# Performance work log

Measured on AMD Instinct MI355X. Metric: run time of the kernel, lower is better.

## Reference

```python
import jax, jax.numpy as jnp
import numpy as np
from jax import lax

B, S, D, H, K = 2, 2048, 1024, 16, 3  # batch, seq, embed, heads, conv kernel
DEPTH = D // H


def silu(x):
    return x * jax.nn.sigmoid(x)


def sep_conv1d(x, dw, pw, b):
    """Keras SeparableConv1D, padding='same', activation=silu.
    x: [B,S,C]; dw: [K,1,C] depthwise kernel; pw: [C,F] pointwise; b: [F]."""
    C = x.shape[-1]
    y = lax.conv_general_dilated(
        x, dw, window_strides=(1,), padding='SAME',
        dimension_numbers=('NWC', 'WIO', 'NWC'), feature_group_count=C)
    y = jnp.einsum('bsc,cf->bsf', y, pw) + b
    return silu(y)


def setup_inputs() -> dict:
    key = jax.random.key(0)
    ks = jax.random.split(key, 20)
    sc = 1.0 / np.sqrt(D)
    inp = {
        'v': jax.random.normal(ks[0], (B, S, D), jnp.float32),
        'k': jax.random.normal(ks[1], (B, S, D), jnp.float32),
        'q': jax.random.normal(ks[2], (B, S, D), jnp.float32),
        'mask': jax.random.randint(ks[3], (B, 1, 1, S), 0, 2, jnp.int32),
        # Dense wq/wk/wv (SiLU)
        'wq_w': jax.random.normal(ks[4], (D, D), jnp.float32) * sc,
        'wq_b': jnp.zeros((D,), jnp.float32),
        'wk_w': jax.random.normal(ks[5], (D, D), jnp.float32) * sc,
        'wk_b': jnp.zeros((D,), jnp.float32),
        'wv_w': jax.random.normal(ks[6], (D, D), jnp.float32) * sc,
        'wv_b': jnp.zeros((D,), jnp.float32),
        # SeparableConv1D params (depthwise [K,1,D], pointwise [D,D], bias [D])
        'dwq': jax.random.normal(ks[7], (K, 1, D), jnp.float32) * 0.1,
        'pwq': jax.random.normal(ks[8], (D, D), jnp.float32) * sc,
        'bq': jnp.zeros((D,), jnp.float32),
        'dwk': jax.random.normal(ks[9], (K, 1, D), jnp.float32) * 0.1,
        'pwk': jax.random.normal(ks[10], (D, D), jnp.float32) * sc,
        'bk': jnp.zeros((D,), jnp.float32),
        'dwv': jax.random.normal(ks[11], (K, 1, D), jnp.float32) * 0.1,
        'pwv': jax.random.normal(ks[12], (D, D), jnp.float32) * sc,
        'bv': jnp.zeros((D,), jnp.float32),
        # output Dense (SiLU)
        'wo_w': jax.random.normal(ks[13], (D, D), jnp.float32) * sc,
        'wo_b': jnp.zeros((D,), jnp.float32),
    }
    return inp


def reference(v, k, q, mask, wq_w, wq_b, wk_w, wk_b, wv_w, wv_b,
              dwq, pwq, bq, dwk, pwk, bk, dwv, pwv, bv, wo_w, wo_b):
    # Dense projections with SiLU
    qp = silu(q @ wq_w + wq_b)
    kp = silu(k @ wk_w + wk_b)
    vp = silu(v @ wv_w + wv_b)
    # SeparableConv1D enhancements (SiLU)
    qc = sep_conv1d(qp, dwq, pwq, bq)
    kc = sep_conv1d(kp, dwk, pwk, bk)
    vc = sep_conv1d(vp, dwv, pwv, bv)
    # split heads -> [B,H,S,depth]
    def split(x):
        return x.reshape(B, S, H, DEPTH).transpose(0, 2, 1, 3)
    qh, kh, vh = split(qc), split(kc), split(vc)
    # scaled dot-product attention with additive mask penalty
    logits = jnp.einsum('bhqd,bhkd->bhqk', qh, kh) / jnp.sqrt(jnp.float32(DEPTH))
    logits = logits + mask.astype(jnp.float32) * -1e9
    attn = jax.nn.softmax(logits, axis=-1)
    out = jnp.einsum('bhqk,bhkd->bhqd', attn, vh)
    out = out.transpose(0, 2, 1, 3).reshape(B, S, D)
    return silu(out @ wo_w + wo_b)
```

## Files before the change

### kernel.cpp

```cpp
#include <hip/hip_runtime.h>
#include <hip/hip_fp16.h>
#include <math.h>

#define BB 2
#define SS 2048
#define DD 1024
#define HH 16
#define MTOT (BB*SS)

typedef _Float16 f16;
typedef _Float16 f16x4 __attribute__((ext_vector_type(4)));
typedef _Float16 f16x8 __attribute__((ext_vector_type(8)));
typedef float    f32x4 __attribute__((ext_vector_type(4)));

#define KSCALE 0.1803368801111204f

__device__ __forceinline__ float silu_f(float x) {
    return x / (1.0f + __expf(-x));
}

__device__ __forceinline__ void gload16(void* lds, const void* g) {
    __builtin_amdgcn_global_load_lds(
        (const __attribute__((address_space(1))) unsigned*)g,
        (__attribute__((address_space(3))) unsigned*)lds, 16, 0, 0);
}

__global__ __launch_bounds__(256) void prep(
    const float* __restrict__ q, const float* __restrict__ k, const float* __restrict__ v,
    f16* __restrict__ x0, f16* __restrict__ x1, f16* __restrict__ x2,
    const float* __restrict__ w0, const float* __restrict__ w1, const float* __restrict__ w2,
    const float* __restrict__ w3, const float* __restrict__ w4, const float* __restrict__ w5,
    const float* __restrict__ w6, f16* __restrict__ wt,
    const int* __restrict__ mask, int* __restrict__ uidx, int* __restrict__ ucnt)
{
    __shared__ float ts[64][65];
    const int gid = blockIdx.x;
    const int t = threadIdx.x;

    if (gid < 6144) {
        const int z = gid >> 11;
        const float* src = z == 0 ? q : z == 1 ? k : v;
        f16* dst = z == 0 ? x0 : z == 1 ? x1 : x2;
        const size_t i8 = ((size_t)(gid & 2047) * 256 + t) * 8;
        const float4 a = *(const float4*)(src + i8);
        const float4 b = *(const float4*)(src + i8 + 4);
        f16x8 h = {(f16)a.x,(f16)a.y,(f16)a.z,(f16)a.w,(f16)b.x,(f16)b.y,(f16)b.z,(f16)b.w};
        *(f16x8*)(dst + i8) = h;
    } else if (gid < 7936) {
        const int w = gid - 6144;
        const int z = w >> 8;
        const int rem = w & 255;
        const int bn = (rem & 15) << 6, bk = (rem >> 4) << 6;
        const float* src;
        switch (z) {
            case 0: src = w0; break; case 1: src = w1; break;
            case 2: src = w2; break; case 3: src = w3; break;
            case 4: src = w4; break; case 5: src = w5; break;
            default: src = w6; break;
        }
        f16* dst = wt + ((size_t)z << 20);
        #pragma unroll
        for (int i = 0; i < 4; ++i) {
            const int fid = t + (i << 8);
            const int r = fid >> 4, c4 = (fid & 15) << 2;
            const float4 v4 = *(const float4*)(src + (size_t)(bk + r) * 1024 + bn + c4);
            ts[r][c4 + 0] = v4.x; ts[r][c4 + 1] = v4.y;
            ts[r][c4 + 2] = v4.z; ts[r][c4 + 3] = v4.w;
        }
        __syncthreads();
        #pragma unroll
        for (int i = 0; i < 4; ++i) {
            const int fid = t + (i << 8);
            const int nr = fid >> 4, k4 = (fid & 15) << 2;
            f16x4 h = { (f16)ts[k4 + 0][nr], (f16)ts[k4 + 1][nr],
                        (f16)ts[k4 + 2][nr], (f16)ts[k4 + 3][nr] };
            *(f16x4*)(dst + (size_t)(bn + nr) * 1024 + bk + k4) = h;
        }
    } else {
        int* ps = (int*)ts;
        const int b = gid - 7936;
        int f[8]; int cnt = 0;
        const int base = b * SS + t * 8;
        #pragma unroll
        for (int j = 0; j < 8; ++j) { f[j] = (mask[base + j] == 0); cnt += f[j]; }
        ps[t] = cnt;
        __syncthreads();
        for (int off = 1; off < 256; off <<= 1) {
            const int pv = (t >= off) ? ps[t - off] : 0;
            __syncthreads();
            ps[t] += pv;
            __syncthreads();
        }
        int pos = ps[t] - cnt;
        #pragma unroll
        for (int j = 0; j < 8; ++j)
            if (f[j]) uidx[b * SS + pos++] = t * 8 + j;
        const int total = ps[255];
        const int pad = (total + 63) & ~63;
        for (int j = total + t; j < pad; j += 256) uidx[b * SS + j] = 0;
        if (t == 0) { ucnt[b * 2] = total; ucnt[b * 2 + 1] = pad; }
    }
}

__global__ __launch_bounds__(256) void dwconv3g(
    const f16* __restrict__ p0, const f16* __restrict__ p1, const f16* __restrict__ p2,
    const float* __restrict__ w0, const float* __restrict__ w1, const float* __restrict__ w2,
    f16* __restrict__ o0, f16* __restrict__ o1, f16* __restrict__ o2)
{
    const int z = blockIdx.y;
    const f16* x = z == 0 ? p0 : z == 1 ? p1 : p2;
    const float* dw = z == 0 ? w0 : z == 1 ? w1 : w2;
    f16* y = z == 0 ? o0 : z == 1 ? o1 : o2;
    const size_t i8 = ((size_t)blockIdx.x * 256 + threadIdx.x) * 8;
    const int c = (int)(i8 % DD);
    const int s = (int)((i8 / DD) % SS);
    const f16x8 xc = *(const f16x8*)(x + i8);
    float acc[8];
    #pragma unroll
    for (int j = 0; j < 8; ++j) acc[j] = (float)xc[j] * dw[DD + c + j];
    if (s > 0) {
        const f16x8 xm = *(const f16x8*)(x + i8 - DD);
        #pragma unroll
        for (int j = 0; j < 8; ++j) acc[j] = fmaf((float)xm[j], dw[c + j], acc[j]);
    }
    if (s < SS - 1) {
        const f16x8 xp = *(const f16x8*)(x + i8 + DD);
        #pragma unroll
        for (int j = 0; j < 8; ++j) acc[j] = fmaf((float)xp[j], dw[2 * DD + c + j], acc[j]);
    }
    f16x8 o;
    #pragma unroll
    for (int j = 0; j < 8; ++j) o[j] = (f16)acc[j];
    *(f16x8*)(y + i8) = o;
}

struct GArg { const f16* A; const f16* W; const float* b; void* C; float scale; };

template<int OUTF32>
__global__ __launch_bounds__(256) void gemm_f16(GArg g0, GArg g1, GArg g2)
{
    __shared__ f16 As[128 * 64];
    __shared__ f16 Bs[128 * 64];

    const GArg ga = blockIdx.z == 0 ? g0 : blockIdx.z == 1 ? g1 : g2;
    const int t = threadIdx.x, l = t & 63, wv = t >> 6;
    const int lr = l & 15, lg = l >> 4;
    const int wr = wv >> 1, wc = wv & 1;

    const int bid = blockIdx.y * 8 + blockIdx.x;
    const int sw = (bid & 7) * 32 + (bid >> 3);
    const int brow = (sw >> 3) << 7, bcol = (sw & 7) << 7;

    const int srow = l >> 3;
    const int schk = (l & 7) ^ (l >> 3);
    const f16* Abase = ga.A + (size_t)(brow + wv * 32 + srow) * 1024 + schk * 8;
    const f16* Bbase = ga.W + (size_t)(bcol + wv * 32 + srow) * 1024 + schk * 8;

    f32x4 acc[4][4];
    #pragma unroll
    for (int m = 0; m < 4; ++m)
        #pragma unroll
        for (int n = 0; n < 4; ++n) acc[m][n] = (f32x4){0.f, 0.f, 0.f, 0.f};

    for (int kt = 0; kt < 16; ++kt) {
        const int k0 = kt << 6;
        #pragma unroll
        for (int j = 0; j < 4; ++j) {
            gload16(As + (wv * 4 + j) * 512, Abase + (size_t)j * 8 * 1024 + k0);
            gload16(Bs + (wv * 4 + j) * 512, Bbase + (size_t)j * 8 * 1024 + k0);
        }
        __syncthreads();

        #pragma unroll
        for (int kk = 0; kk < 2; ++kk) {
            f16x8 af[4], bf[4];
            #pragma unroll
            for (int m = 0; m < 4; ++m) {
                const int row = (wr << 6) + (m << 4) + lr;
                const int off = row * 128 + ((((kk << 6) | (lg << 4))) ^ ((lr & 7) << 4));
                af[m] = *(const f16x8*)((const char*)As + off);
            }
            #pragma unroll
            for (int n = 0; n < 4; ++n) {
                const int row = (wc << 6) + (n << 4) + lr;
                const int off = row * 128 + ((((kk << 6) | (lg << 4))) ^ ((lr & 7) << 4));
                bf[n] = *(const f16x8*)((const char*)Bs + off);
            }
            #pragma unroll
            for (int m = 0; m < 4; ++m)
                #pragma unroll
                for (int n = 0; n < 4; ++n)
                    acc[m][n] = __builtin_amdgcn_mfma_f32_16x16x32_f16(af[m], bf[n], acc[m][n], 0, 0, 0);
        }
        __syncthreads();
    }

    float bv[4];
    #pragma unroll
    for (int n = 0; n < 4; ++n) bv[n] = ga.b[bcol + (wc << 6) + (n << 4) + lr];
    #pragma unroll
    for (int m = 0; m < 4; ++m)
        #pragma unroll
        for (int n = 0; n < 4; ++n)
            #pragma unroll
            for (int i = 0; i < 4; ++i) {
                const int row = brow + (wr << 6) + (m << 4) + (lg << 2) + i;
                const int col = bcol + (wc << 6) + (n << 4) + lr;
                const float o = silu_f(acc[m][n][i] + bv[n]) * ga.scale;
                if (OUTF32) ((float*)ga.C)[(size_t)row * 1024 + col] = o;
                else        ((f16*)ga.C)[(size_t)row * 1024 + col] = (f16)o;
            }
}

__global__ __launch_bounds__(512) void gemm256(GArg g0, GArg g1, GArg g2)
{
    __shared__ f16 As[256 * 64];
    __shared__ f16 Bs[128 * 64];

    const GArg ga = blockIdx.z == 0 ? g0 : blockIdx.z == 1 ? g1 : g2;
    const int t = threadIdx.x, l = t & 63, wv = t >> 6;
    const int lr = l & 15, lg = l >> 4;
    const int wm = wv >> 1, wn = wv & 1;

    const int bid = blockIdx.y * 8 + blockIdx.x;
    const int sw = (bid & 7) * 16 + (bid >> 3);
    const int brow = (sw >> 3) << 8;
    const int bcol = (sw & 7) << 7;

    const int srow = l >> 3;
    const int schk = (l & 7) ^ (l >> 3);
    const f16* Abase = ga.A + (size_t)(brow + wv * 32 + srow) * 1024 + schk * 8;
    const f16* Bbase = ga.W + (size_t)(bcol + wv * 16 + srow) * 1024 + schk * 8;

    f32x4 acc[4][4];
    #pragma unroll
    for (int m = 0; m < 4; ++m)
        #pragma unroll
        for (int n = 0; n < 4; ++n) acc[m][n] = (f32x4){0.f, 0.f, 0.f, 0.f};

    for (int kt = 0; kt < 16; ++kt) {
        const int k0 = kt << 6;
        #pragma unroll
        for (int j = 0; j < 4; ++j)
            gload16(As + (wv * 4 + j) * 512, Abase + (size_t)j * 8 * 1024 + k0);
        #pragma unroll
        for (int j = 0; j < 2; ++j)
            gload16(Bs + (wv * 2 + j) * 512, Bbase + (size_t)j * 8 * 1024 + k0);
        __syncthreads();

        #pragma unroll
        for (int kk = 0; kk < 2; ++kk) {
            f16x8 af[4], bf[4];
            #pragma unroll
            for (int m = 0; m < 4; ++m) {
                const int row = (wm << 6) + (m << 4) + lr;
                const int off = row * 128 + ((((kk << 6) | (lg << 4))) ^ ((lr & 7) << 4));
                af[m] = *(const f16x8*)((const char*)As + off);
            }
            #pragma unroll
            for (int n = 0; n < 4; ++n) {
                const int row = (wn << 6) + (n << 4) + lr;
                const int off = row * 128 + ((((kk << 6) | (lg << 4))) ^ ((lr & 7) << 4));
                bf[n] = *(const f16x8*)((const char*)Bs + off);
            }
            #pragma unroll
            for (int m = 0; m < 4; ++m)
                #pragma unroll
                for (int n = 0; n < 4; ++n)
                    acc[m][n] = __builtin_amdgcn_mfma_f32_16x16x32_f16(af[m], bf[n], acc[m][n], 0, 0, 0);
        }
        __syncthreads();
    }

    float bv[4];
    #pragma unroll
    for (int n = 0; n < 4; ++n) bv[n] = ga.b[bcol + (wn << 6) + (n << 4) + lr];
    #pragma unroll
    for (int m = 0; m < 4; ++m)
        #pragma unroll
        for (int n = 0; n < 4; ++n)
            #pragma unroll
            for (int i = 0; i < 4; ++i) {
                const int row = brow + (wm << 6) + (m << 4) + (lg << 2) + i;
                const int col = bcol + (wn << 6) + (n << 4) + lr;
                const float o = silu_f(acc[m][n][i] + bv[n]) * ga.scale;
                ((f16*)ga.C)[(size_t)row * 1024 + col] = (f16)o;
            }
}

__global__ __launch_bounds__(512) void attn_f16(
    const f16* __restrict__ Q, const f16* __restrict__ Kf,
    const f16* __restrict__ Vf, const int* __restrict__ uidx,
    const int* __restrict__ ucnt, f16* __restrict__ O)
{
    __shared__ f16 Ks[2 * 64 * 64];
    __shared__ f16 Vt[2 * 64 * 64];
    __shared__ f16 Pw[8 * 16 * 64];
    __shared__ int uix[2048];

    const int t = threadIdx.x;
    const int l = t & 63, wv = t >> 6;
    const int lr = l & 15, lg = l >> 4;

    const int bid = blockIdx.x;
    const int sw = (bid & 7) * 64 + (bid >> 3);
    const int qb = (sw & 15) << 7;
    const int h  = (sw >> 4) & 15;
    const int b  = sw >> 8;

    const int cnt = ucnt[b * 2];
    const int pad = ucnt[b * 2 + 1];

    const int srow = l >> 3;
    const int schk = (l & 7) ^ (l >> 3);

    const int bkv = (t & 15) << 2;
    const int bnv = (t >> 4) << 2;

    for (int j = t; j < 2048; j += 512) uix[j] = uidx[b * SS + j];

    const size_t bbase = (size_t)b * SS;
    const size_t qrow = bbase + qb + (wv << 4) + lr;
    const f16x8 aq0 = *(const f16x8*)(Q + qrow * DD + h * 64 + (lg << 3));
    const f16x8 aq1 = *(const f16x8*)(Q + qrow * DD + h * 64 + 32 + (lg << 3));

    float m_s = -1e30f, l_s = 0.f;
    f32x4 acc[4];
    #pragma unroll
    for (int n = 0; n < 4; ++n) acc[n] = (f32x4){0.f, 0.f, 0.f, 0.f};

    const int rdswz = (lr & 7) << 4;
    const int poff = (wv << 11) + lr * 128;

    __syncthreads();

#define PROCESS(TB, KT) do {                                                  \
    const int kb = (TB) * 8192;                                               \
    f16x8 bk0[4], bk1[4];                                                     \
    _Pragma("unroll")                                                         \
    for (int n = 0; n < 4; ++n) {                                             \
        const int row = (n << 4) + lr;                                        \
        bk0[n] = *(const f16x8*)((const char*)Ks + kb + row * 128 + (((lg << 4)) ^ rdswz));        \
        bk1[n] = *(const f16x8*)((const char*)Ks + kb + row * 128 + (((64) | (lg << 4)) ^ rdswz)); \
    }                                                                         \
    const bool full = ((KT) + 64 <= cnt);                                     \
                 \
    f32x4 s[4];                                                               \
    __builtin_amdgcn_s_setprio(1);                                            \
    _Pragma("unroll")                                                         \
    for (int n = 0; n < 4; ++n) {                                             \
        f32x4 z = (f32x4){0.f, 0.f, 0.f, 0.f};                                \
        z = __builtin_amdgcn_mfma_f32_16x16x32_f16(bk0[n], aq0, z, 0, 0, 0);  \
        z = __builtin_amdgcn_mfma_f32_16x16x32_f16(bk1[n], aq1, z, 0, 0, 0);  \
        if (full) {                                                           \
            _Pragma("unroll")                                                 \
            for (int i = 0; i < 4; ++i) s[n][i] = z[i];                       \
        } else {                                                              \
            _Pragma("unroll")                                                 \
            for (int i = 0; i < 4; ++i) {                                     \
                const bool valid = ((KT) + (n << 4) + (lg << 2) + i) < cnt;   \
                s[n][i] = valid ? z[i] : -1e30f;                              \
            }                                                                 \
        }                                                                     \
    }                                                                         \
    __builtin_amdgcn_s_setprio(0);                                            \
                   \
    float pm = s[0][0];                                                       \
    _Pragma("unroll")                                                         \
    for (int n = 0; n < 4; ++n)                                               \
        _Pragma("unroll")                                                     \
        for (int i = 0; i < 4; ++i) pm = fmaxf(pm, s[n][i]);                  \
    if (!__all(pm - m_s <= 8.0f)) {           \
        float pr = pm;                                                        \
        pr = fmaxf(pr, __shfl_xor(pr, 16));                                   \
        pr = fmaxf(pr, __shfl_xor(pr, 32));                                   \
        const float mn = fmaxf(m_s, pr);                                      \
        const float sc = exp2f(m_s - mn);                                     \
        m_s = mn;                                                             \
        l_s *= sc;                                                            \
        _Pragma("unroll")                                                     \
        for (int n = 0; n < 4; ++n)                                           \
            _Pragma("unroll")                                                 \
            for (int i = 0; i < 4; ++i) acc[n][i] *= sc;                      \
    }                                                                         \
      \
    _Pragma("unroll")                                                         \
    for (int n = 0; n < 4; ++n) {                                             \
        f16x4 p4;                                                             \
        _Pragma("unroll")                                                     \
        for (int i = 0; i < 4; ++i) {                                         \
            const float p = exp2f(s[n][i] - m_s);         \
            l_s += p;                                                         \
            p4[i] = (f16)p;                                                   \
        }                                                                     \
        const int off = poff + (((n << 5) | (lg << 3)) ^ rdswz);              \
        *(f16x4*)((char*)Pw + off) = p4;                                      \
    }                                                                         \
             \
    {                                                                         \
        const f16x8 pb0 = *(const f16x8*)((const char*)Pw + poff + (((lg << 4)) ^ rdswz));        \
        const f16x8 pb1 = *(const f16x8*)((const char*)Pw + poff + (((64) | (lg << 4)) ^ rdswz)); \
        __builtin_amdgcn_s_setprio(1);                                        \
        _Pragma("unroll")                                                     \
        for (int n = 0; n < 4; ++n) {                                         \
            const int row = (n << 4) + lr;                                    \
            const f16x8 av0 = *(const f16x8*)((const char*)Vt + kb + row * 128 + (((lg << 4)) ^ rdswz));        \
            const f16x8 av1 = *(const f16x8*)((const char*)Vt + kb + row * 128 + (((64) | (lg << 4)) ^ rdswz)); \
            acc[n] = __builtin_amdgcn_mfma_f32_16x16x32_f16(av0, pb0, acc[n], 0, 0, 0);  \
            acc[n] = __builtin_amdgcn_mfma_f32_16x16x32_f16(av1, pb1, acc[n], 0, 0, 0);  \
        }                                                                     \
        __builtin_amdgcn_s_setprio(0);                                        \
    }                                                                         \
} while (0)

    for (int kt = 0; kt < pad; kt += 128) {
        const bool two = (kt + 64) < pad;
        {
            const int krow0 = uix[kt + wv * 8 + srow];
            gload16(Ks + wv * 512, Kf + (bbase + krow0) * DD + h * 64 + schk * 8);
            if (two) {
                const int krow1 = uix[kt + 64 + wv * 8 + srow];
                gload16(Ks + 4096 + wv * 512, Kf + (bbase + krow1) * DD + h * 64 + schk * 8);
            }
        }
        if (t < 256) {
            const int nhalf = two ? 2 : 1;
            for (int half = 0; half < nhalf; ++half) {
                f16x4 vl[4];
                #pragma unroll
                for (int r = 0; r < 4; ++r) {
                    const int vrow = uix[kt + half * 64 + bkv + r];
                    vl[r] = *(const f16x4*)(Vf + (bbase + vrow) * DD + h * 64 + bnv);
                }
                #pragma unroll
                for (int j = 0; j < 4; ++j) {
                    f16x4 h4 = { vl[0][j], vl[1][j], vl[2][j], vl[3][j] };
                    const int row = bnv + j;
                    const int off = half * 8192 + row * 128 + ((bkv * 2) ^ ((row & 7) << 4));
                    *(f16x4*)((char*)Vt + off) = h4;
                }
            }
        }
        __syncthreads();

        PROCESS(0, kt);
        if (two) PROCESS(1, kt + 64);

        __syncthreads();
    }
#undef PROCESS

    l_s += __shfl_xor(l_s, 16);
    l_s += __shfl_xor(l_s, 32);
    const float inv = 1.0f / l_s;
    const size_t orow = bbase + qb + (wv << 4) + lr;
    #pragma unroll
    for (int n = 0; n < 4; ++n) {
        f16x4 o4;
        #pragma unroll
        for (int i = 0; i < 4; ++i) o4[i] = (f16)(acc[n][i] * inv);
        *(f16x4*)(O + orow * DD + h * 64 + (n << 4) + (lg << 2)) = o4;
    }
}

extern "C" void kernel_launch(void* const* d_in, const int* in_sizes, int n_in,
                              void* d_out, int out_size, void* d_ws, size_t ws_size,
                              hipStream_t stream) {
    const float* v    = (const float*)d_in[0];
    const float* k    = (const float*)d_in[1];
    const float* q    = (const float*)d_in[2];
    const int*   mask = (const int*)  d_in[3];
    const float* wq_w = (const float*)d_in[4];
    const float* wq_b = (const float*)d_in[5];
    const float* wk_w = (const float*)d_in[6];
    const float* wk_b = (const float*)d_in[7];
    const float* wv_w = (const float*)d_in[8];
    const float* wv_b = (const float*)d_in[9];
    const float* dwq  = (const float*)d_in[10];
    const float* pwq  = (const float*)d_in[11];
    const float* bq   = (const float*)d_in[12];
    const float* dwk  = (const float*)d_in[13];
    const float* pwk  = (const float*)d_in[14];
    const float* bk   = (const float*)d_in[15];
    const float* dwv  = (const float*)d_in[16];
    const float* pwv  = (const float*)d_in[17];
    const float* bv   = (const float*)d_in[18];
    const float* wo_w = (const float*)d_in[19];
    const float* wo_b = (const float*)d_in[20];
    float* out = (float*)d_out;

    const size_t NE = (size_t)MTOT * DD;
    f16* wt = (f16*)d_ws;
    f16* x0 = wt + 7 * (size_t)(1 << 20);
    f16* x1 = x0 + NE;
    f16* x2 = x1 + NE;
    f16* p0 = x2 + NE;
    f16* p1 = p0 + NE;
    f16* p2 = p1 + NE;
    f16* ao = p2 + NE;
    int* uidx = (int*)(ao + NE);
    int* ucnt = uidx + MTOT;

    f16* wtq = wt,              *wtk = wt + (1u<<20), *wtv = wt + 2*(1u<<20);
    f16* wpq = wt + 3*(1u<<20), *wpk = wt + 4*(1u<<20), *wpv = wt + 5*(1u<<20);
    f16* wto = wt + 6*(1u<<20);

    prep<<<dim3(7938), 256, 0, stream>>>(q, k, v, x0, x1, x2,
        wq_w, wk_w, wv_w, pwq, pwk, pwv, wo_w, wt, mask, uidx, ucnt);
    gemm256<<<dim3(8, 16, 3), 512, 0, stream>>>(
        GArg{x0, wtq, wq_b, p0, 1.0f}, GArg{x1, wtk, wk_b, p1, 1.0f},
        GArg{x2, wtv, wv_b, p2, 1.0f});
    dwconv3g<<<dim3(2048, 3), 256, 0, stream>>>(p0, p1, p2, dwq, dwk, dwv, x0, x1, x2);
    gemm256<<<dim3(8, 16, 3), 512, 0, stream>>>(
        GArg{x0, wpq, bq, p0, 1.0f}, GArg{x1, wpk, bk, p1, KSCALE},
        GArg{x2, wpv, bv, p2, 1.0f});
    attn_f16<<<dim3(512), 512, 0, stream>>>(p0, p1, p2, uidx, ucnt, ao);
    gemm_f16<1><<<dim3(8, 32, 1), 256, 0, stream>>>(
        GArg{ao, wto, wo_b, out, 1.0f}, GArg{ao, wto, wo_b, out, 1.0f},
        GArg{ao, wto, wo_b, out, 1.0f});
}
```

Baseline: 175.8 us.

## Gather unmasked K/V rows in pointwise GEMM and skip masked tiles

The pointwise-conv GEMM for K and V now gathers only unmasked rows through the compacted index list, writes them densely and returns early for row tiles past the padded count. Attention then reads K/V contiguously, with no per-row index indirection and no LDS index buffer. The output projection now uses the 256-row GEMM template with an fp32 store path instead of the separate 128-tile kernel. This roughly halves the K/V pointwise GEMM work for a random mask and simplifies attention loads. The trade-off is gathered A-row loads in the GEMM.

```diff
diff --git a/kernel.cpp b/kernel.cpp
--- a/kernel.cpp
+++ b/kernel.cpp
@@ -97,7 +97,7 @@
             if (f[j]) uidx[b * SS + pos++] = t * 8 + j;
         const int total = ps[255];
         const int pad = (total + 63) & ~63;
-        for (int j = total + t; j < pad; j += 256) uidx[b * SS + j] = 0;
+        for (int j = total + t; j < SS; j += 256) uidx[b * SS + j] = 0;
         if (t == 0) { ucnt[b * 2] = total; ucnt[b * 2 + 1] = pad; }
     }
 }
@@ -134,85 +134,11 @@
     *(f16x8*)(y + i8) = o;
 }
 
-struct GArg { const f16* A; const f16* W; const float* b; void* C; float scale; };
+struct GArg { const f16* A; const f16* W; const float* b; void* C; float scale; int gather; };
 
 template<int OUTF32>
-__global__ __launch_bounds__(256) void gemm_f16(GArg g0, GArg g1, GArg g2)
-{
-    __shared__ f16 As[128 * 64];
-    __shared__ f16 Bs[128 * 64];
-
-    const GArg ga = blockIdx.z == 0 ? g0 : blockIdx.z == 1 ? g1 : g2;
-    const int t = threadIdx.x, l = t & 63, wv = t >> 6;
-    const int lr = l & 15, lg = l >> 4;
-    const int wr = wv >> 1, wc = wv & 1;
-
-    const int bid = blockIdx.y * 8 + blockIdx.x;
-    const int sw = (bid & 7) * 32 + (bid >> 3);
-    const int brow = (sw >> 3) << 7, bcol = (sw & 7) << 7;
-
-    const int srow = l >> 3;
-    const int schk = (l & 7) ^ (l >> 3);
-    const f16* Abase = ga.A + (size_t)(brow + wv * 32 + srow) * 1024 + schk * 8;
-    const f16* Bbase = ga.W + (size_t)(bcol + wv * 32 + srow) * 1024 + schk * 8;
-
-    f32x4 acc[4][4];
-    #pragma unroll
-    for (int m = 0; m < 4; ++m)
-        #pragma unroll
-        for (int n = 0; n < 4; ++n) acc[m][n] = (f32x4){0.f, 0.f, 0.f, 0.f};
-
-    for (int kt = 0; kt < 16; ++kt) {
-        const int k0 = kt << 6;
-        #pragma unroll
-        for (int j = 0; j < 4; ++j) {
-            gload16(As + (wv * 4 + j) * 512, Abase + (size_t)j * 8 * 1024 + k0);
-            gload16(Bs + (wv * 4 + j) * 512, Bbase + (size_t)j * 8 * 1024 + k0);
-        }
-        __syncthreads();
-
-        #pragma unroll
-        for (int kk = 0; kk < 2; ++kk) {
-            f16x8 af[4], bf[4];
-            #pragma unroll
-            for (int m = 0; m < 4; ++m) {
-                const int row = (wr << 6) + (m << 4) + lr;
-                const int off = row * 128 + ((((kk << 6) | (lg << 4))) ^ ((lr & 7) << 4));
-                af[m] = *(const f16x8*)((const char*)As + off);
-            }
-            #pragma unroll
-            for (int n = 0; n < 4; ++n) {
-                const int row = (wc << 6) + (n << 4) + lr;
-                const int off = row * 128 + ((((kk << 6) | (lg << 4))) ^ ((lr & 7) << 4));
-                bf[n] = *(const f16x8*)((const char*)Bs + off);
-            }
-            #pragma unroll
-            for (int m = 0; m < 4; ++m)
-                #pragma unroll
-                for (int n = 0; n < 4; ++n)
-                    acc[m][n] = __builtin_amdgcn_mfma_f32_16x16x32_f16(af[m], bf[n], acc[m][n], 0, 0, 0);
-        }
-        __syncthreads();
-    }
-
-    float bv[4];
-    #pragma unroll
-    for (int n = 0; n < 4; ++n) bv[n] = ga.b[bcol + (wc << 6) + (n << 4) + lr];
-    #pragma unroll
-    for (int m = 0; m < 4; ++m)
-        #pragma unroll
-        for (int n = 0; n < 4; ++n)
-            #pragma unroll
-            for (int i = 0; i < 4; ++i) {
-                const int row = brow + (wr << 6) + (m << 4) + (lg << 2) + i;
-                const int col = bcol + (wc << 6) + (n << 4) + lr;
-                const float o = silu_f(acc[m][n][i] + bv[n]) * ga.scale;
-                if (OUTF32) ((float*)ga.C)[(size_t)row * 1024 + col] = o;
-                else        ((f16*)ga.C)[(size_t)row * 1024 + col] = (f16)o;
-            }
-}
-
-__global__ __launch_bounds__(512) void gemm256(GArg g0, GArg g1, GArg g2)
+__global__ __launch_bounds__(512) void gemm256(GArg g0, GArg g1, GArg g2,
+    const int* __restrict__ uidx, const int* __restrict__ ucnt)
 {
     __shared__ f16 As[256 * 64];
     __shared__ f16 Bs[128 * 64];
@@ -227,9 +153,21 @@
     const int brow = (sw >> 3) << 8;
     const int bcol = (sw & 7) << 7;
 
+    const int b = brow >> 11;
+    if (ga.gather) {
+        if ((brow & 2047) >= ucnt[b * 2 + 1]) return;
+    }
+
     const int srow = l >> 3;
     const int schk = (l & 7) ^ (l >> 3);
-    const f16* Abase = ga.A + (size_t)(brow + wv * 32 + srow) * 1024 + schk * 8;
+
+    const f16* Aptr[4];
+    #pragma unroll
+    for (int j = 0; j < 4; ++j) {
+        int r = (brow & 2047) + wv * 32 + j * 8 + srow;
+        if (ga.gather) r = uidx[b * SS + r];
+        Aptr[j] = ga.A + ((size_t)(b << 11) + r) * 1024 + schk * 8;
+    }
     const f16* Bbase = ga.W + (size_t)(bcol + wv * 16 + srow) * 1024 + schk * 8;
 
     f32x4 acc[4][4];
@@ -242,7 +180,7 @@
         const int k0 = kt << 6;
         #pragma unroll
         for (int j = 0; j < 4; ++j)
-            gload16(As + (wv * 4 + j) * 512, Abase + (size_t)j * 8 * 1024 + k0);
+            gload16(As + (wv * 4 + j) * 512, Aptr[j] + k0);
         #pragma unroll
         for (int j = 0; j < 2; ++j)
             gload16(Bs + (wv * 2 + j) * 512, Bbase + (size_t)j * 8 * 1024 + k0);
@@ -284,19 +222,19 @@
                 const int row = brow + (wm << 6) + (m << 4) + (lg << 2) + i;
                 const int col = bcol + (wn << 6) + (n << 4) + lr;
                 const float o = silu_f(acc[m][n][i] + bv[n]) * ga.scale;
-                ((f16*)ga.C)[(size_t)row * 1024 + col] = (f16)o;
+                if (OUTF32) ((float*)ga.C)[(size_t)row * 1024 + col] = o;
+                else        ((f16*)ga.C)[(size_t)row * 1024 + col] = (f16)o;
             }
 }
 
 __global__ __launch_bounds__(512) void attn_f16(
     const f16* __restrict__ Q, const f16* __restrict__ Kf,
-    const f16* __restrict__ Vf, const int* __restrict__ uidx,
-    const int* __restrict__ ucnt, f16* __restrict__ O)
+    const f16* __restrict__ Vf, const int* __restrict__ ucnt,
+    f16* __restrict__ O)
 {
     __shared__ f16 Ks[2 * 64 * 64];
     __shared__ f16 Vt[2 * 64 * 64];
     __shared__ f16 Pw[8 * 16 * 64];
-    __shared__ int uix[2048];
 
     const int t = threadIdx.x;
     const int l = t & 63, wv = t >> 6;
@@ -317,8 +255,6 @@
     const int bkv = (t & 15) << 2;
     const int bnv = (t >> 4) << 2;
 
-    for (int j = t; j < 2048; j += 512) uix[j] = uidx[b * SS + j];
-
     const size_t bbase = (size_t)b * SS;
     const size_t qrow = bbase + qb + (wv << 4) + lr;
     const f16x8 aq0 = *(const f16x8*)(Q + qrow * DD + h * 64 + (lg << 3));
@@ -331,8 +267,6 @@
 
     const int rdswz = (lr & 7) << 4;
     const int poff = (wv << 11) + lr * 128;
-
-    __syncthreads();
 
 #define PROCESS(TB, KT) do {                                                  \
     const int kb = (TB) * 8192;                                               \
@@ -364,7 +298,6 @@
         }                                                                     \
     }                                                                         \
     __builtin_amdgcn_s_setprio(0);                                            \
-                   \
     float pm = s[0][0];                                                       \
     _Pragma("unroll")                                                         \
     for (int n = 0; n < 4; ++n)                                               \
@@ -383,7 +316,6 @@
             _Pragma("unroll")                                                 \
             for (int i = 0; i < 4; ++i) acc[n][i] *= sc;                      \
     }                                                                         \
-      \
     _Pragma("unroll")                                                         \
     for (int n = 0; n < 4; ++n) {                                             \
         f16x4 p4;                                                             \
@@ -396,7 +328,6 @@
         const int off = poff + (((n << 5) | (lg << 3)) ^ rdswz);              \
         *(f16x4*)((char*)Pw + off) = p4;                                      \
     }                                                                         \
-             \
     {                                                                         \
         const f16x8 pb0 = *(const f16x8*)((const char*)Pw + poff + (((lg << 4)) ^ rdswz));        \
         const f16x8 pb1 = *(const f16x8*)((const char*)Pw + poff + (((64) | (lg << 4)) ^ rdswz)); \
@@ -415,23 +346,18 @@
 
     for (int kt = 0; kt < pad; kt += 128) {
         const bool two = (kt + 64) < pad;
-        {
-            const int krow0 = uix[kt + wv * 8 + srow];
-            gload16(Ks + wv * 512, Kf + (bbase + krow0) * DD + h * 64 + schk * 8);
-            if (two) {
-                const int krow1 = uix[kt + 64 + wv * 8 + srow];
-                gload16(Ks + 4096 + wv * 512, Kf + (bbase + krow1) * DD + h * 64 + schk * 8);
-            }
-        }
+        gload16(Ks + wv * 512,
+                Kf + (bbase + kt + wv * 8 + srow) * DD + h * 64 + schk * 8);
+        if (two)
+            gload16(Ks + 4096 + wv * 512,
+                    Kf + (bbase + kt + 64 + wv * 8 + srow) * DD + h * 64 + schk * 8);
         if (t < 256) {
             const int nhalf = two ? 2 : 1;
             for (int half = 0; half < nhalf; ++half) {
                 f16x4 vl[4];
                 #pragma unroll
-                for (int r = 0; r < 4; ++r) {
-                    const int vrow = uix[kt + half * 64 + bkv + r];
-                    vl[r] = *(const f16x4*)(Vf + (bbase + vrow) * DD + h * 64 + bnv);
-                }
+                for (int r = 0; r < 4; ++r)
+                    vl[r] = *(const f16x4*)(Vf + (bbase + kt + half * 64 + bkv + r) * DD + h * 64 + bnv);
                 #pragma unroll
                 for (int j = 0; j < 4; ++j) {
                     f16x4 h4 = { vl[0][j], vl[1][j], vl[2][j], vl[3][j] };
@@ -507,15 +433,15 @@
 
     prep<<<dim3(7938), 256, 0, stream>>>(q, k, v, x0, x1, x2,
         wq_w, wk_w, wv_w, pwq, pwk, pwv, wo_w, wt, mask, uidx, ucnt);
-    gemm256<<<dim3(8, 16, 3), 512, 0, stream>>>(
-        GArg{x0, wtq, wq_b, p0, 1.0f}, GArg{x1, wtk, wk_b, p1, 1.0f},
-        GArg{x2, wtv, wv_b, p2, 1.0f});
+    gemm256<0><<<dim3(8, 16, 3), 512, 0, stream>>>(
+        GArg{x0, wtq, wq_b, p0, 1.0f, 0}, GArg{x1, wtk, wk_b, p1, 1.0f, 0},
+        GArg{x2, wtv, wv_b, p2, 1.0f, 0}, uidx, ucnt);
     dwconv3g<<<dim3(2048, 3), 256, 0, stream>>>(p0, p1, p2, dwq, dwk, dwv, x0, x1, x2);
-    gemm256<<<dim3(8, 16, 3), 512, 0, stream>>>(
-        GArg{x0, wpq, bq, p0, 1.0f}, GArg{x1, wpk, bk, p1, KSCALE},
-        GArg{x2, wpv, bv, p2, 1.0f});
-    attn_f16<<<dim3(512), 512, 0, stream>>>(p0, p1, p2, uidx, ucnt, ao);
-    gemm_f16<1><<<dim3(8, 32, 1), 256, 0, stream>>>(
-        GArg{ao, wto, wo_b, out, 1.0f}, GArg{ao, wto, wo_b, out, 1.0f},
-        GArg{ao, wto, wo_b, out, 1.0f});
-}
+    gemm256<0><<<dim3(8, 16, 3), 512, 0, stream>>>(
+        GArg{x0, wpq, bq, p0, 1.0f, 0}, GArg{x1, wpk, bk, p1, KSCALE, 1},
+        GArg{x2, wpv, bv, p2, 1.0f, 1}, uidx, ucnt);
+    attn_f16<<<dim3(512), 512, 0, stream>>>(p0, p1, p2, ucnt, ao);
+    gemm256<1><<<dim3(8, 16, 1), 512, 0, stream>>>(
+        GArg{ao, wto, wo_b, out, 1.0f, 0}, GArg{ao, wto, wo_b, out, 1.0f, 0},
+        GArg{ao, wto, wo_b, out, 1.0f, 0}, uidx, ucnt);
+}
```

Result: no change. 177.3 us (+0.9%).

## Compact unmasked K/V rows in pointwise GEMM and process two Q tiles per wave

Applied to the files above, without the earlier changes.

The pointwise-conv GEMM for K and V now gathers only unmasked rows through the index list and writes them densely, skipping row tiles past the padded count. Attention then reads K and V contiguously instead of through per-row indirection in LDS. Each wave now handles 32 query rows (two 16-row sub-tiles) and reuses the K/V LDS fragments for both, so the grid halves to 256 blocks. The trade-offs are lower occupancy and parallelism, higher register pressure, and padding indices now filled out to the full sequence length.

```diff
diff --git a/kernel.cpp b/kernel.cpp
--- a/kernel.cpp
+++ b/kernel.cpp
@@ -97,7 +97,7 @@
             if (f[j]) uidx[b * SS + pos++] = t * 8 + j;
         const int total = ps[255];
         const int pad = (total + 63) & ~63;
-        for (int j = total + t; j < pad; j += 256) uidx[b * SS + j] = 0;
+        for (int j = total + t; j < SS; j += 256) uidx[b * SS + j] = 0;
         if (t == 0) { ucnt[b * 2] = total; ucnt[b * 2 + 1] = pad; }
     }
 }
@@ -134,7 +134,7 @@
     *(f16x8*)(y + i8) = o;
 }
 
-struct GArg { const f16* A; const f16* W; const float* b; void* C; float scale; };
+struct GArg { const f16* A; const f16* W; const float* b; void* C; float scale; int gather; };
 
 template<int OUTF32>
 __global__ __launch_bounds__(256) void gemm_f16(GArg g0, GArg g1, GArg g2)
@@ -212,7 +212,9 @@
             }
 }
 
-__global__ __launch_bounds__(512) void gemm256(GArg g0, GArg g1, GArg g2)
+template<int OUTF32>
+__global__ __launch_bounds__(512) void gemm256(GArg g0, GArg g1, GArg g2,
+    const int* __restrict__ uidx, const int* __restrict__ ucnt)
 {
     __shared__ f16 As[256 * 64];
     __shared__ f16 Bs[128 * 64];
@@ -227,9 +229,21 @@
     const int brow = (sw >> 3) << 8;
     const int bcol = (sw & 7) << 7;
 
+    const int b = brow >> 11;
+    if (ga.gather) {
+        if ((brow & 2047) >= ucnt[b * 2 + 1]) return;
+    }
+
     const int srow = l >> 3;
     const int schk = (l & 7) ^ (l >> 3);
-    const f16* Abase = ga.A + (size_t)(brow + wv * 32 + srow) * 1024 + schk * 8;
+
+    const f16* Aptr[4];
+    #pragma unroll
+    for (int j = 0; j < 4; ++j) {
+        int r = (brow & 2047) + wv * 32 + j * 8 + srow;
+        if (ga.gather) r = uidx[b * SS + r];
+        Aptr[j] = ga.A + ((size_t)(b << 11) + r) * 1024 + schk * 8;
+    }
     const f16* Bbase = ga.W + (size_t)(bcol + wv * 16 + srow) * 1024 + schk * 8;
 
     f32x4 acc[4][4];
@@ -242,7 +256,7 @@
         const int k0 = kt << 6;
         #pragma unroll
         for (int j = 0; j < 4; ++j)
-            gload16(As + (wv * 4 + j) * 512, Abase + (size_t)j * 8 * 1024 + k0);
+            gload16(As + (wv * 4 + j) * 512, Aptr[j] + k0);
         #pragma unroll
         for (int j = 0; j < 2; ++j)
             gload16(Bs + (wv * 2 + j) * 512, Bbase + (size_t)j * 8 * 1024 + k0);
@@ -284,29 +298,29 @@
                 const int row = brow + (wm << 6) + (m << 4) + (lg << 2) + i;
                 const int col = bcol + (wn << 6) + (n << 4) + lr;
                 const float o = silu_f(acc[m][n][i] + bv[n]) * ga.scale;
-                ((f16*)ga.C)[(size_t)row * 1024 + col] = (f16)o;
+                if (OUTF32) ((float*)ga.C)[(size_t)row * 1024 + col] = o;
+                else        ((f16*)ga.C)[(size_t)row * 1024 + col] = (f16)o;
             }
 }
 
 __global__ __launch_bounds__(512) void attn_f16(
     const f16* __restrict__ Q, const f16* __restrict__ Kf,
-    const f16* __restrict__ Vf, const int* __restrict__ uidx,
-    const int* __restrict__ ucnt, f16* __restrict__ O)
+    const f16* __restrict__ Vf, const int* __restrict__ ucnt,
+    f16* __restrict__ O)
 {
     __shared__ f16 Ks[2 * 64 * 64];
     __shared__ f16 Vt[2 * 64 * 64];
     __shared__ f16 Pw[8 * 16 * 64];
-    __shared__ int uix[2048];
 
     const int t = threadIdx.x;
     const int l = t & 63, wv = t >> 6;
     const int lr = l & 15, lg = l >> 4;
 
     const int bid = blockIdx.x;
-    const int sw = (bid & 7) * 64 + (bid >> 3);
-    const int qb = (sw & 15) << 7;
-    const int h  = (sw >> 4) & 15;
-    const int b  = sw >> 8;
+    const int sw = (bid & 7) * 32 + (bid >> 3);
+    const int qb = (sw & 7) << 8;
+    const int h  = (sw >> 3) & 15;
+    const int b  = sw >> 7;
 
     const int cnt = ucnt[b * 2];
     const int pad = ucnt[b * 2 + 1];
@@ -314,44 +328,35 @@
     const int srow = l >> 3;
     const int schk = (l & 7) ^ (l >> 3);
 
-    const int bkv = (t & 15) << 2;
-    const int bnv = (t >> 4) << 2;
-
-    for (int j = t; j < 2048; j += 512) uix[j] = uidx[b * SS + j];
+    const int th  = t & 255;
+    const int vhalf = t >> 8;
+    const int bkv = (th & 15) << 2;
+    const int bnv = (th >> 4) << 2;
 
     const size_t bbase = (size_t)b * SS;
-    const size_t qrow = bbase + qb + (wv << 4) + lr;
-    const f16x8 aq0 = *(const f16x8*)(Q + qrow * DD + h * 64 + (lg << 3));
-    const f16x8 aq1 = *(const f16x8*)(Q + qrow * DD + h * 64 + 32 + (lg << 3));
-
-    float m_s = -1e30f, l_s = 0.f;
-    f32x4 acc[4];
-    #pragma unroll
-    for (int n = 0; n < 4; ++n) acc[n] = (f32x4){0.f, 0.f, 0.f, 0.f};
+    const size_t qrowA = bbase + qb + (wv << 5) + lr;
+    const size_t qrowB = qrowA + 16;
+    const f16x8 aqA0 = *(const f16x8*)(Q + qrowA * DD + h * 64 + (lg << 3));
+    const f16x8 aqA1 = *(const f16x8*)(Q + qrowA * DD + h * 64 + 32 + (lg << 3));
+    const f16x8 aqB0 = *(const f16x8*)(Q + qrowB * DD + h * 64 + (lg << 3));
+    const f16x8 aqB1 = *(const f16x8*)(Q + qrowB * DD + h * 64 + 32 + (lg << 3));
+
+    float mA = -1e30f, lA = 0.f, mB = -1e30f, lB = 0.f;
+    f32x4 accA[4], accB[4];
+    #pragma unroll
+    for (int n = 0; n < 4; ++n) { accA[n] = (f32x4){0.f,0.f,0.f,0.f}; accB[n] = (f32x4){0.f,0.f,0.f,0.f}; }
 
     const int rdswz = (lr & 7) << 4;
     const int poff = (wv << 11) + lr * 128;
 
-    __syncthreads();
-
-#define PROCESS(TB, KT) do {                                                  \
-    const int kb = (TB) * 8192;                                               \
-    f16x8 bk0[4], bk1[4];                                                     \
-    _Pragma("unroll")                                                         \
-    for (int n = 0; n < 4; ++n) {                                             \
-        const int row = (n << 4) + lr;                                        \
-        bk0[n] = *(const f16x8*)((const char*)Ks + kb + row * 128 + (((lg << 4)) ^ rdswz));        \
-        bk1[n] = *(const f16x8*)((const char*)Ks + kb + row * 128 + (((64) | (lg << 4)) ^ rdswz)); \
-    }                                                                         \
-    const bool full = ((KT) + 64 <= cnt);                                     \
-                 \
+#define SUBPROC(AQ0, AQ1, M_, L_, ACC_, KT) do {                              \
     f32x4 s[4];                                                               \
     __builtin_amdgcn_s_setprio(1);                                            \
     _Pragma("unroll")                                                         \
     for (int n = 0; n < 4; ++n) {                                             \
         f32x4 z = (f32x4){0.f, 0.f, 0.f, 0.f};                                \
-        z = __builtin_amdgcn_mfma_f32_16x16x32_f16(bk0[n], aq0, z, 0, 0, 0);  \
-        z = __builtin_amdgcn_mfma_f32_16x16x32_f16(bk1[n], aq1, z, 0, 0, 0);  \
+        z = __builtin_amdgcn_mfma_f32_16x16x32_f16(bk0[n], AQ0, z, 0, 0, 0);  \
+        z = __builtin_amdgcn_mfma_f32_16x16x32_f16(bk1[n], AQ1, z, 0, 0, 0);  \
         if (full) {                                                           \
             _Pragma("unroll")                                                 \
             for (int i = 0; i < 4; ++i) s[n][i] = z[i];                       \
@@ -364,50 +369,44 @@
         }                                                                     \
     }                                                                         \
     __builtin_amdgcn_s_setprio(0);                                            \
-                   \
     float pm = s[0][0];                                                       \
     _Pragma("unroll")                                                         \
     for (int n = 0; n < 4; ++n)                                               \
         _Pragma("unroll")                                                     \
         for (int i = 0; i < 4; ++i) pm = fmaxf(pm, s[n][i]);                  \
-    if (!__all(pm - m_s <= 8.0f)) {           \
+    if (!__all(pm - M_ <= 8.0f)) {            \
         float pr = pm;                                                        \
         pr = fmaxf(pr, __shfl_xor(pr, 16));                                   \
         pr = fmaxf(pr, __shfl_xor(pr, 32));                                   \
-        const float mn = fmaxf(m_s, pr);                                      \
-        const float sc = exp2f(m_s - mn);                                     \
-        m_s = mn;                                                             \
-        l_s *= sc;                                                            \
+        const float mn = fmaxf(M_, pr);                                       \
+        const float sc = exp2f(M_ - mn);                                      \
+        M_ = mn;                                                              \
+        L_ *= sc;                                                             \
         _Pragma("unroll")                                                     \
         for (int n = 0; n < 4; ++n)                                           \
             _Pragma("unroll")                                                 \
-            for (int i = 0; i < 4; ++i) acc[n][i] *= sc;                      \
+            for (int i = 0; i < 4; ++i) ACC_[n][i] *= sc;                     \
     }                                                                         \
-      \
     _Pragma("unroll")                                                         \
     for (int n = 0; n < 4; ++n) {                                             \
         f16x4 p4;                                                             \
         _Pragma("unroll")                                                     \
         for (int i = 0; i < 4; ++i) {                                         \
-            const float p = exp2f(s[n][i] - m_s);         \
-            l_s += p;                                                         \
+            const float p = exp2f(s[n][i] - M_);          \
+            L_ += p;                                                          \
             p4[i] = (f16)p;                                                   \
         }                                                                     \
         const int off = poff + (((n << 5) | (lg << 3)) ^ rdswz);              \
         *(f16x4*)((char*)Pw + off) = p4;                                      \
     }                                                                         \
-             \
     {                                                                         \
         const f16x8 pb0 = *(const f16x8*)((const char*)Pw + poff + (((lg << 4)) ^ rdswz));        \
         const f16x8 pb1 = *(const f16x8*)((const char*)Pw + poff + (((64) | (lg << 4)) ^ rdswz)); \
         __builtin_amdgcn_s_setprio(1);                                        \
         _Pragma("unroll")                                                     \
         for (int n = 0; n < 4; ++n) {                                         \
-            const int row = (n << 4) + lr;                                    \
-            const f16x8 av0 = *(const f16x8*)((const char*)Vt + kb + row * 128 + (((lg << 4)) ^ rdswz));        \
-            const f16x8 av1 = *(const f16x8*)((const char*)Vt + kb + row * 128 + (((64) | (lg << 4)) ^ rdswz)); \
-            acc[n] = __builtin_amdgcn_mfma_f32_16x16x32_f16(av0, pb0, acc[n], 0, 0, 0);  \
-            acc[n] = __builtin_amdgcn_mfma_f32_16x16x32_f16(av1, pb1, acc[n], 0, 0, 0);  \
+            ACC_[n] = __builtin_amdgcn_mfma_f32_16x16x32_f16(av0[n], pb0, ACC_[n], 0, 0, 0);  \
+            ACC_[n] = __builtin_amdgcn_mfma_f32_16x16x32_f16(av1[n], pb1, ACC_[n], 0, 0, 0);  \
         }                                                                     \
         __builtin_amdgcn_s_setprio(0);                                        \
     }                                                                         \
@@ -415,51 +414,64 @@
 
     for (int kt = 0; kt < pad; kt += 128) {
         const bool two = (kt + 64) < pad;
-        {
-            const int krow0 = uix[kt + wv * 8 + srow];
-            gload16(Ks + wv * 512, Kf + (bbase + krow0) * DD + h * 64 + schk * 8);
-            if (two) {
-                const int krow1 = uix[kt + 64 + wv * 8 + srow];
-                gload16(Ks + 4096 + wv * 512, Kf + (bbase + krow1) * DD + h * 64 + schk * 8);
-            }
-        }
-        if (t < 256) {
-            const int nhalf = two ? 2 : 1;
-            for (int half = 0; half < nhalf; ++half) {
-                f16x4 vl[4];
-                #pragma unroll
-                for (int r = 0; r < 4; ++r) {
-                    const int vrow = uix[kt + half * 64 + bkv + r];
-                    vl[r] = *(const f16x4*)(Vf + (bbase + vrow) * DD + h * 64 + bnv);
-                }
-                #pragma unroll
-                for (int j = 0; j < 4; ++j) {
-                    f16x4 h4 = { vl[0][j], vl[1][j], vl[2][j], vl[3][j] };
-                    const int row = bnv + j;
-                    const int off = half * 8192 + row * 128 + ((bkv * 2) ^ ((row & 7) << 4));
-                    *(f16x4*)((char*)Vt + off) = h4;
-                }
-            }
-        }
-        __syncthreads();
-
-        PROCESS(0, kt);
-        if (two) PROCESS(1, kt + 64);
-
-        __syncthreads();
-    }
-#undef PROCESS
-
-    l_s += __shfl_xor(l_s, 16);
-    l_s += __shfl_xor(l_s, 32);
-    const float inv = 1.0f / l_s;
-    const size_t orow = bbase + qb + (wv << 4) + lr;
+        gload16(Ks + wv * 512,
+                Kf + (bbase + kt + wv * 8 + srow) * DD + h * 64 + schk * 8);
+        if (two)
+            gload16(Ks + 4096 + wv * 512,
+                    Kf + (bbase + kt + 64 + wv * 8 + srow) * DD + h * 64 + schk * 8);
+        if (vhalf == 0 || two) {
+            f16x4 vl[4];
+            #pragma unroll
+            for (int r = 0; r < 4; ++r)
+                vl[r] = *(const f16x4*)(Vf + (bbase + kt + vhalf * 64 + bkv + r) * DD + h * 64 + bnv);
+            #pragma unroll
+            for (int j = 0; j < 4; ++j) {
+                f16x4 h4 = { vl[0][j], vl[1][j], vl[2][j], vl[3][j] };
+                const int row = bnv + j;
+                const int off = vhalf * 8192 + row * 128 + ((bkv * 2) ^ ((row & 7) << 4));
+                *(f16x4*)((char*)Vt + off) = h4;
+            }
+        }
+        __syncthreads();
+
+        #pragma unroll 1
+        for (int tb = 0; tb < 2; ++tb) {
+            if (tb == 1 && !two) break;
+            const int kb = tb * 8192;
+            const int kt0 = kt + tb * 64;
+            f16x8 bk0[4], bk1[4], av0[4], av1[4];
+            #pragma unroll
+            for (int n = 0; n < 4; ++n) {
+                const int row = (n << 4) + lr;
+                bk0[n] = *(const f16x8*)((const char*)Ks + kb + row * 128 + (((lg << 4)) ^ rdswz));
+                bk1[n] = *(const f16x8*)((const char*)Ks + kb + row * 128 + (((64) | (lg << 4)) ^ rdswz));
+                av0[n] = *(const f16x8*)((const char*)Vt + kb + row * 128 + (((lg << 4)) ^ rdswz));
+                av1[n] = *(const f16x8*)((const char*)Vt + kb + row * 128 + (((64) | (lg << 4)) ^ rdswz));
+            }
+            const bool full = (kt0 + 64 <= cnt);
+            SUBPROC(aqA0, aqA1, mA, lA, accA, kt0);
+            SUBPROC(aqB0, aqB1, mB, lB, accB, kt0);
+        }
+
+        __syncthreads();
+    }
+#undef SUBPROC
+
+    lA += __shfl_xor(lA, 16);
+    lA += __shfl_xor(lA, 32);
+    lB += __shfl_xor(lB, 16);
+    lB += __shfl_xor(lB, 32);
+    const float invA = 1.0f / lA, invB = 1.0f / lB;
     #pragma unroll
     for (int n = 0; n < 4; ++n) {
-        f16x4 o4;
-        #pragma unroll
-        for (int i = 0; i < 4; ++i) o4[i] = (f16)(acc[n][i] * inv);
-        *(f16x4*)(O + orow * DD + h * 64 + (n << 4) + (lg << 2)) = o4;
+        f16x4 oA, oB;
+        #pragma unroll
+        for (int i = 0; i < 4; ++i) {
+            oA[i] = (f16)(accA[n][i] * invA);
+            oB[i] = (f16)(accB[n][i] * invB);
+        }
+        *(f16x4*)(O + qrowA * DD + h * 64 + (n << 4) + (lg << 2)) = oA;
+        *(f16x4*)(O + qrowB * DD + h * 64 + (n << 4) + (lg << 2)) = oB;
     }
 }
 
@@ -507,15 +519,15 @@
 
     prep<<<dim3(7938), 256, 0, stream>>>(q, k, v, x0, x1, x2,
         wq_w, wk_w, wv_w, pwq, pwk, pwv, wo_w, wt, mask, uidx, ucnt);
-    gemm256<<<dim3(8, 16, 3), 512, 0, stream>>>(
-        GArg{x0, wtq, wq_b, p0, 1.0f}, GArg{x1, wtk, wk_b, p1, 1.0f},
-        GArg{x2, wtv, wv_b, p2, 1.0f});
+    gemm256<0><<<dim3(8, 16, 3), 512, 0, stream>>>(
+        GArg{x0, wtq, wq_b, p0, 1.0f, 0}, GArg{x1, wtk, wk_b, p1, 1.0f, 0},
+        GArg{x2, wtv, wv_b, p2, 1.0f, 0}, uidx, ucnt);
     dwconv3g<<<dim3(2048, 3), 256, 0, stream>>>(p0, p1, p2, dwq, dwk, dwv, x0, x1, x2);
-    gemm256<<<dim3(8, 16, 3), 512, 0, stream>>>(
-        GArg{x0, wpq, bq, p0, 1.0f}, GArg{x1, wpk, bk, p1, KSCALE},
-        GArg{x2, wpv, bv, p2, 1.0f});
-    attn_f16<<<dim3(512), 512, 0, stream>>>(p0, p1, p2, uidx, ucnt, ao);
+    gemm256<0><<<dim3(8, 16, 3), 512, 0, stream>>>(
+        GArg{x0, wpq, bq, p0, 1.0f, 0}, GArg{x1, wpk, bk, p1, KSCALE, 1},
+        GArg{x2, wpv, bv, p2, 1.0f, 1}, uidx, ucnt);
+    attn_f16<<<dim3(256), 512, 0, stream>>>(p0, p1, p2, ucnt, ao);
     gemm_f16<1><<<dim3(8, 32, 1), 256, 0, stream>>>(
-        GArg{ao, wto, wo_b, out, 1.0f}, GArg{ao, wto, wo_b, out, 1.0f},
-        GArg{ao, wto, wo_b, out, 1.0f});
-}
+        GArg{ao, wto, wo_b, out, 1.0f, 0}, GArg{ao, wto, wo_b, out, 1.0f, 0},
+        GArg{ao, wto, wo_b, out, 1.0f, 0});
+}
```

New measurement: 182.2 us. +3.7%, slower.

## Gather unmasked key rows in pointwise GEMM and compact K/V for attention

Applied to the files above, without the earlier changes.

The pointwise-conv GEMM for K and V now gathers only unmasked sequence rows through uidx and writes them compactly, skipping row tiles past the padded count. Attention then reads K and V contiguously instead of through an LDS index table, which removes the uix staging, one barrier and the indirect loads. This cuts roughly half of the K/V pointwise GEMM work under the random mask. The cost is indirect A-row addressing in the GEMM and a wider zero-fill of uidx.

```diff
diff --git a/kernel.cpp b/kernel.cpp
--- a/kernel.cpp
+++ b/kernel.cpp
@@ -97,7 +97,7 @@
             if (f[j]) uidx[b * SS + pos++] = t * 8 + j;
         const int total = ps[255];
         const int pad = (total + 63) & ~63;
-        for (int j = total + t; j < pad; j += 256) uidx[b * SS + j] = 0;
+        for (int j = total + t; j < SS; j += 256) uidx[b * SS + j] = 0;
         if (t == 0) { ucnt[b * 2] = total; ucnt[b * 2 + 1] = pad; }
     }
 }
@@ -134,7 +134,7 @@
     *(f16x8*)(y + i8) = o;
 }
 
-struct GArg { const f16* A; const f16* W; const float* b; void* C; float scale; };
+struct GArg { const f16* A; const f16* W; const float* b; void* C; float scale; int gather; };
 
 template<int OUTF32>
 __global__ __launch_bounds__(256) void gemm_f16(GArg g0, GArg g1, GArg g2)
@@ -212,7 +212,9 @@
             }
 }
 
-__global__ __launch_bounds__(512) void gemm256(GArg g0, GArg g1, GArg g2)
+template<int OUTF32>
+__global__ __launch_bounds__(512) void gemm256(GArg g0, GArg g1, GArg g2,
+    const int* __restrict__ uidx, const int* __restrict__ ucnt)
 {
     __shared__ f16 As[256 * 64];
     __shared__ f16 Bs[128 * 64];
@@ -227,9 +229,21 @@
     const int brow = (sw >> 3) << 8;
     const int bcol = (sw & 7) << 7;
 
+    const int b = brow >> 11;
+    if (ga.gather) {
+        if ((brow & 2047) >= ucnt[b * 2 + 1]) return;
+    }
+
     const int srow = l >> 3;
     const int schk = (l & 7) ^ (l >> 3);
-    const f16* Abase = ga.A + (size_t)(brow + wv * 32 + srow) * 1024 + schk * 8;
+
+    const f16* Aptr[4];
+    #pragma unroll
+    for (int j = 0; j < 4; ++j) {
+        int r = (brow & 2047) + wv * 32 + j * 8 + srow;
+        if (ga.gather) r = uidx[b * SS + r];
+        Aptr[j] = ga.A + ((size_t)(b << 11) + r) * 1024 + schk * 8;
+    }
     const f16* Bbase = ga.W + (size_t)(bcol + wv * 16 + srow) * 1024 + schk * 8;
 
     f32x4 acc[4][4];
@@ -242,7 +256,7 @@
         const int k0 = kt << 6;
         #pragma unroll
         for (int j = 0; j < 4; ++j)
-            gload16(As + (wv * 4 + j) * 512, Abase + (size_t)j * 8 * 1024 + k0);
+            gload16(As + (wv * 4 + j) * 512, Aptr[j] + k0);
         #pragma unroll
         for (int j = 0; j < 2; ++j)
             gload16(Bs + (wv * 2 + j) * 512, Bbase + (size_t)j * 8 * 1024 + k0);
@@ -284,19 +298,19 @@
                 const int row = brow + (wm << 6) + (m << 4) + (lg << 2) + i;
                 const int col = bcol + (wn << 6) + (n << 4) + lr;
                 const float o = silu_f(acc[m][n][i] + bv[n]) * ga.scale;
-                ((f16*)ga.C)[(size_t)row * 1024 + col] = (f16)o;
+                if (OUTF32) ((float*)ga.C)[(size_t)row * 1024 + col] = o;
+                else        ((f16*)ga.C)[(size_t)row * 1024 + col] = (f16)o;
             }
 }
 
 __global__ __launch_bounds__(512) void attn_f16(
     const f16* __restrict__ Q, const f16* __restrict__ Kf,
-    const f16* __restrict__ Vf, const int* __restrict__ uidx,
-    const int* __restrict__ ucnt, f16* __restrict__ O)
+    const f16* __restrict__ Vf, const int* __restrict__ ucnt,
+    f16* __restrict__ O)
 {
     __shared__ f16 Ks[2 * 64 * 64];
     __shared__ f16 Vt[2 * 64 * 64];
     __shared__ f16 Pw[8 * 16 * 64];
-    __shared__ int uix[2048];
 
     const int t = threadIdx.x;
     const int l = t & 63, wv = t >> 6;
@@ -317,8 +331,6 @@
     const int bkv = (t & 15) << 2;
     const int bnv = (t >> 4) << 2;
 
-    for (int j = t; j < 2048; j += 512) uix[j] = uidx[b * SS + j];
-
     const size_t bbase = (size_t)b * SS;
     const size_t qrow = bbase + qb + (wv << 4) + lr;
     const f16x8 aq0 = *(const f16x8*)(Q + qrow * DD + h * 64 + (lg << 3));
@@ -331,8 +343,6 @@
 
     const int rdswz = (lr & 7) << 4;
     const int poff = (wv << 11) + lr * 128;
-
-    __syncthreads();
 
 #define PROCESS(TB, KT) do {                                                  \
     const int kb = (TB) * 8192;                                               \
@@ -364,7 +374,6 @@
         }                                                                     \
     }                                                                         \
     __builtin_amdgcn_s_setprio(0);                                            \
-                   \
     float pm = s[0][0];                                                       \
     _Pragma("unroll")                                                         \
     for (int n = 0; n < 4; ++n)                                               \
@@ -383,7 +392,6 @@
             _Pragma("unroll")                                                 \
             for (int i = 0; i < 4; ++i) acc[n][i] *= sc;                      \
     }                                                                         \
-      \
     _Pragma("unroll")                                                         \
     for (int n = 0; n < 4; ++n) {                                             \
         f16x4 p4;                                                             \
@@ -396,7 +404,6 @@
         const int off = poff + (((n << 5) | (lg << 3)) ^ rdswz);              \
         *(f16x4*)((char*)Pw + off) = p4;                                      \
     }                                                                         \
-             \
     {                                                                         \
         const f16x8 pb0 = *(const f16x8*)((const char*)Pw + poff + (((lg << 4)) ^ rdswz));        \
         const f16x8 pb1 = *(const f16x8*)((const char*)Pw + poff + (((64) | (lg << 4)) ^ rdswz)); \
@@ -415,23 +422,18 @@
 
     for (int kt = 0; kt < pad; kt += 128) {
         const bool two = (kt + 64) < pad;
-        {
-            const int krow0 = uix[kt + wv * 8 + srow];
-            gload16(Ks + wv * 512, Kf + (bbase + krow0) * DD + h * 64 + schk * 8);
-            if (two) {
-                const int krow1 = uix[kt + 64 + wv * 8 + srow];
-                gload16(Ks + 4096 + wv * 512, Kf + (bbase + krow1) * DD + h * 64 + schk * 8);
-            }
-        }
+        gload16(Ks + wv * 512,
+                Kf + (bbase + kt + wv * 8 + srow) * DD + h * 64 + schk * 8);
+        if (two)
+            gload16(Ks + 4096 + wv * 512,
+                    Kf + (bbase + kt + 64 + wv * 8 + srow) * DD + h * 64 + schk * 8);
         if (t < 256) {
             const int nhalf = two ? 2 : 1;
             for (int half = 0; half < nhalf; ++half) {
                 f16x4 vl[4];
                 #pragma unroll
-                for (int r = 0; r < 4; ++r) {
-                    const int vrow = uix[kt + half * 64 + bkv + r];
-                    vl[r] = *(const f16x4*)(Vf + (bbase + vrow) * DD + h * 64 + bnv);
-                }
+                for (int r = 0; r < 4; ++r)
+                    vl[r] = *(const f16x4*)(Vf + (bbase + kt + half * 64 + bkv + r) * DD + h * 64 + bnv);
                 #pragma unroll
                 for (int j = 0; j < 4; ++j) {
                     f16x4 h4 = { vl[0][j], vl[1][j], vl[2][j], vl[3][j] };
@@ -507,15 +509,15 @@
 
     prep<<<dim3(7938), 256, 0, stream>>>(q, k, v, x0, x1, x2,
         wq_w, wk_w, wv_w, pwq, pwk, pwv, wo_w, wt, mask, uidx, ucnt);
-    gemm256<<<dim3(8, 16, 3), 512, 0, stream>>>(
-        GArg{x0, wtq, wq_b, p0, 1.0f}, GArg{x1, wtk, wk_b, p1, 1.0f},
-        GArg{x2, wtv, wv_b, p2, 1.0f});
+    gemm256<0><<<dim3(8, 16, 3), 512, 0, stream>>>(
+        GArg{x0, wtq, wq_b, p0, 1.0f, 0}, GArg{x1, wtk, wk_b, p1, 1.0f, 0},
+        GArg{x2, wtv, wv_b, p2, 1.0f, 0}, uidx, ucnt);
     dwconv3g<<<dim3(2048, 3), 256, 0, stream>>>(p0, p1, p2, dwq, dwk, dwv, x0, x1, x2);
-    gemm256<<<dim3(8, 16, 3), 512, 0, stream>>>(
-        GArg{x0, wpq, bq, p0, 1.0f}, GArg{x1, wpk, bk, p1, KSCALE},
-        GArg{x2, wpv, bv, p2, 1.0f});
-    attn_f16<<<dim3(512), 512, 0, stream>>>(p0, p1, p2, uidx, ucnt, ao);
+    gemm256<0><<<dim3(8, 16, 3), 512, 0, stream>>>(
+        GArg{x0, wpq, bq, p0, 1.0f, 0}, GArg{x1, wpk, bk, p1, KSCALE, 1},
+        GArg{x2, wpv, bv, p2, 1.0f, 1}, uidx, ucnt);
+    attn_f16<<<dim3(512), 512, 0, stream>>>(p0, p1, p2, ucnt, ao);
     gemm_f16<1><<<dim3(8, 32, 1), 256, 0, stream>>>(
-        GArg{ao, wto, wo_b, out, 1.0f}, GArg{ao, wto, wo_b, out, 1.0f},
-        GArg{ao, wto, wo_b, out, 1.0f});
-}
+        GArg{ao, wto, wo_b, out, 1.0f, 0}, GArg{ao, wto, wo_b, out, 1.0f, 0},
+        GArg{ao, wto, wo_b, out, 1.0f, 0});
+}
```

Result: no change. 173.6 us, median of 3 (-1.2%).
